# Optimization experiments

Hardware: AMD Instinct MI355X
Metric: run time of the kernel (lower is better)

## Reference

```python
import jax, jax.numpy as jnp
import numpy as np

VOCAB_LIST = np.array([16384, 2048, 256], dtype=np.int64)
SIZES = VOCAB_LIST + 1                       # +1 level-mask token per level
LEVEL_ENDS = jnp.asarray(np.cumsum(SIZES))   # [3] cumulative vocab ends
MASK_TOKENS = LEVEL_ENDS - 1                 # level mask token ids
TOTAL_V = int(SIZES.sum())                   # 18691
N_LAYER, N_EMBD, N_HEAD = 4, 1024, 16
HEAD_DIM = N_EMBD // N_HEAD
FF = 4 * N_EMBD
MEMORY_SPAN = 256
SOFTCAP = 30.0


def rms_norm(x):
    return x * jax.lax.rsqrt(jnp.mean(x * x, axis=-1, keepdims=True) + 1e-6)


def rotary(x):
    # x: [B, S, H, D]; half-split rotation as in modded-nanogpt
    S, D = x.shape[1], x.shape[-1]
    half = D // 2
    inv_freq = 1.0 / (10000.0 ** (jnp.arange(half, dtype=jnp.float32) / half))
    freqs = jnp.outer(jnp.arange(S, dtype=jnp.float32), inv_freq)  # [S, half]
    cos = jnp.cos(freqs)[None, :, None, :]
    sin = jnp.sin(freqs)[None, :, None, :]
    x1, x2 = x[..., :half], x[..., half:]
    return jnp.concatenate([x1 * cos + x2 * sin, -x1 * sin + x2 * cos], axis=-1)


def build_mask(levels):
    # keep kv if causal AND (kv is a higher-level 'global' token OR within recent window)
    S = levels.shape[1]
    q = jnp.arange(S)[:, None]
    k = jnp.arange(S)[None, :]
    causal = q >= k
    recent = (q - k) <= MEMORY_SPAN
    higher = (levels > 0)[:, None, :]                 # [B,1,S]
    return causal[None] & (higher | recent[None])     # [B,S,S]


def forward(idx, target, wte, lambdas, lamb, wq, wk, wv, wo, w1, w2, lm_head):
    B, S = idx.shape
    levels = jnp.searchsorted(LEVEL_ENDS, idx, side='right')   # infer_level
    mask = build_mask(levels)[:, None]                         # [B,1,S,S]
    x = rms_norm(wte[idx])
    x0 = x
    v1 = None
    for i in range(N_LAYER):
        xr = lambdas[i, 0] * x + lambdas[i, 1] * x0
        h = rms_norm(xr)
        q = (h @ wq[i].T).reshape(B, S, N_HEAD, HEAD_DIM)
        k = (h @ wk[i].T).reshape(B, S, N_HEAD, HEAD_DIM)
        v = (h @ wv[i].T).reshape(B, S, N_HEAD, HEAD_DIM)
        if v1 is None:
            v1 = v                                  # value residual from layer 0
        v = (1.0 - lamb[i]) * v + lamb[i] * v1
        q = rotary(rms_norm(q))                     # QK-norm then rotary
        k = rotary(rms_norm(k))
        scores = jnp.einsum('bqhd,bkhd->bhqk', q, k) / jnp.sqrt(jnp.float32(HEAD_DIM))
        scores = jnp.where(mask, scores, -jnp.inf)
        attn = jax.nn.softmax(scores, axis=-1)
        y = jnp.einsum('bhqk,bkhd->bqhd', attn, v).reshape(B, S, N_EMBD)
        x = xr + y @ wo[i].T
        m = rms_norm(x)
        x = x + (jax.nn.relu(m @ w1[i].T) ** 2) @ w2[i].T   # ReLU^2 MLP
    x = rms_norm(x)
    logits = x @ lm_head.T
    logits = SOFTCAP * jnp.tanh(logits / SOFTCAP)
    logp = jax.nn.log_softmax(logits.astype(jnp.float32), axis=-1)
    loss = -jnp.take_along_axis(logp, target[..., None].astype(jnp.int32), axis=-1)[..., 0]
    loss = jnp.where(jnp.isin(target, MASK_TOKENS), 0.0, loss)
    return loss


def setup_inputs() -> dict:
    key = jax.random.key(0)
    ks = jax.random.split(key, 12)
    B, S, D, V, F, L = 2, 2048, N_EMBD, TOTAL_V, FF, N_LAYER
    s = 0.02
    return {
        'idx': jax.random.randint(ks[0], (B, S), 0, V, dtype=jnp.int32),
        'target': jax.random.randint(ks[1], (B, S), 0, V, dtype=jnp.int32),
        'wte': jax.random.normal(ks[2], (V, D), dtype=jnp.float32),
        'lambdas': jnp.tile(jnp.array([1.0, 0.0], dtype=jnp.float32), (L, 1)),
        'lamb': jnp.full((L,), 0.5, dtype=jnp.float32),
        'wq': jax.random.normal(ks[3], (L, D, D), dtype=jnp.float32) * s,
        'wk': jax.random.normal(ks[4], (L, D, D), dtype=jnp.float32) * s,
        'wv': jax.random.normal(ks[5], (L, D, D), dtype=jnp.float32) * s,
        'wo': jax.random.normal(ks[6], (L, D, D), dtype=jnp.float32) * s,
        'w1': jax.random.normal(ks[7], (L, F, D), dtype=jnp.float32) * s,
        'w2': jax.random.normal(ks[8], (L, D, F), dtype=jnp.float32) * s,
        'lm_head': jax.random.normal(ks[9], (V, D), dtype=jnp.float32) * 0.01,
    }


def reference(idx, target, wte, lambdas, lamb, wq, wk, wv, wo, w1, w2, lm_head):
    return forward(idx, target, wte, lambdas, lamb, wq, wk, wv, wo, w1, w2, lm_head)
```

## Files before the change

### kernel.cpp

```cpp
#include <hip/hip_runtime.h>
#include <hip/hip_bf16.h>

#define TT 4096
#define SS 2048
#define BBATCH 2
#define DM 1024
#define NH 16
#define HD 64
#define FFD 4096
#define NL 4
#define VV 18691
#define VP 18816
#define APITCH 72
#define NXLM 147
#define SENT 0x3FFFFFFF

typedef __bf16 bf16x8 __attribute__((ext_vector_type(8)));
typedef float f32x4 __attribute__((ext_vector_type(4)));
typedef const __attribute__((address_space(1))) void* gas_t;
typedef __attribute__((address_space(3))) void* las_t;

__device__ __forceinline__ float bfb2f(unsigned short u) {
    union { unsigned int i; float f; } x;
    x.i = ((unsigned int)u) << 16;
    return x.f;
}
__device__ __forceinline__ unsigned short f2bfb(float f) {
    union { float f; unsigned int i; } x;
    x.f = f;
    unsigned int r = 0x7fffu + ((x.i >> 16) & 1u);
    x.i += r;
    return (unsigned short)(x.i >> 16);
}

__device__ __forceinline__ float wave_sum(float v) {
#pragma unroll
    for (int o = 32; o; o >>= 1) v += __shfl_xor(v, o, 64);
    return v;
}

__device__ __forceinline__ float block_sum256(float v) {
    __shared__ float sb[4];
    v = wave_sum(v);
    int wid = threadIdx.x >> 6;
    if ((threadIdx.x & 63) == 0) sb[wid] = v;
    __syncthreads();
    float t = sb[0] + sb[1] + sb[2] + sb[3];
    __syncthreads();
    return t;
}

__global__ __launch_bounds__(256) void cvtw_kernel(const float* __restrict__ src,
                                                   unsigned short* __restrict__ dst, int n)
{
    int i = (blockIdx.x * 256 + threadIdx.x) * 4;
    if (i >= n) return;
    float4 f = *reinterpret_cast<const float4*>(src + i);
    ushort4 u;
    u.x = f2bfb(f.x); u.y = f2bfb(f.y); u.z = f2bfb(f.z); u.w = f2bfb(f.w);
    *reinterpret_cast<ushort4*>(dst + i) = u;
}

__global__ __launch_bounds__(256) void cvtpad_kernel(const float* __restrict__ src,
                                                     unsigned short* __restrict__ dst,
                                                     int nreal, int ntot)
{
    int i = (blockIdx.x * 256 + threadIdx.x) * 4;
    if (i >= ntot) return;
    ushort4 u = {0, 0, 0, 0};
    if (i < nreal) {
        float4 f = *reinterpret_cast<const float4*>(src + i);
        u.x = f2bfb(f.x); u.y = f2bfb(f.y); u.z = f2bfb(f.z); u.w = f2bfb(f.w);
    }
    *reinterpret_cast<ushort4*>(dst + i) = u;
}

__global__ __launch_bounds__(256) void ropetab_kernel(float2* __restrict__ tab)
{
    int s = blockIdx.x * 8 + (threadIdx.x >> 5);
    int j = threadIdx.x & 31;
    float invf = exp2f(-(float)j * 0.41524101186092025f);
    float ang = (float)s * invf;
    float sn, cs;
    sincosf(ang, &sn, &cs);
    tab[s * 32 + j] = make_float2(cs, sn);
}

__global__ __launch_bounds__(256) void embed_kernel(
    const int* __restrict__ idx, const float* __restrict__ wte,
    float* __restrict__ x, unsigned short* __restrict__ x0, int* __restrict__ levels)
{
    int t = blockIdx.x;
    int id = idx[t];
    const float* row = wte + (size_t)id * DM;
    float4 v = *reinterpret_cast<const float4*>(row + threadIdx.x * 4);
    float ss = v.x * v.x + v.y * v.y + v.z * v.z + v.w * v.w;
    float tot = block_sum256(ss);
    float rs = rsqrtf(tot / (float)DM + 1e-6f);
    float4 o;
    o.x = v.x * rs; o.y = v.y * rs; o.z = v.z * rs; o.w = v.w * rs;
    size_t off = (size_t)t * DM + threadIdx.x * 4;
    *reinterpret_cast<float4*>(x + off) = o;
    ushort4 ub;
    ub.x = f2bfb(o.x); ub.y = f2bfb(o.y); ub.z = f2bfb(o.z); ub.w = f2bfb(o.w);
    *reinterpret_cast<ushort4*>(x0 + off) = ub;
    if (threadIdx.x == 0) levels[t] = (id >= 16385) + (id >= 18434);
}

__global__ __launch_bounds__(256) void pack_kernel(
    const int* __restrict__ levels, int* __restrict__ gpos, int* __restrict__ nbuf)
{
    int b = blockIdx.x;
    const int* lv = levels + b * SS;
    int* gp = gpos + b * SS;
    __shared__ int wsum[4];
    __shared__ int base;
    if (threadIdx.x == 0) base = 0;
    __syncthreads();
    int lane = threadIdx.x & 63, w = threadIdx.x >> 6;
    for (int c = 0; c < SS; c += 256) {
        int s = c + threadIdx.x;
        int flag = (lv[s] > 0) ? 1 : 0;
        unsigned long long mask = __ballot(flag);
        int pre = __popcll(mask & ((1ull << lane) - 1ull));
        int wtot = __popcll(mask);
        if (lane == 0) wsum[w] = wtot;
        __syncthreads();
        int woff = 0;
#pragma unroll
        for (int i = 0; i < 4; ++i) if (i < w) woff += wsum[i];
        int tot = wsum[0] + wsum[1] + wsum[2] + wsum[3];
        int mybase = base;
        if (flag) gp[mybase + woff + pre] = s;
        __syncthreads();
        if (threadIdx.x == 0) base += tot;
        __syncthreads();
    }
    int nb = base;
    int nbp = (nb + 63) & ~63;
    for (int i = nb + threadIdx.x; i < SS; i += 256) gp[i] = SENT;
    if (threadIdx.x == 0) { nbuf[b] = nb; nbuf[BBATCH + b] = nbp; }
}

__global__ __launch_bounds__(64) void gather_kernel(
    const unsigned short* __restrict__ kb, const unsigned short* __restrict__ vb,
    const int* __restrict__ gpos, const int* __restrict__ nbuf,
    unsigned short* __restrict__ kp, unsigned short* __restrict__ vp)
{
    int b = blockIdx.x >> 11;
    int j = blockIdx.x & (SS - 1);
    if (j >= nbuf[BBATCH + b]) return;
    int pos = gpos[b * SS + j];
    int lane = threadIdx.x;
    size_t dst = ((size_t)b * SS + j) * DM + lane * 16;
    if (pos < SS) {
        size_t src = ((size_t)b * SS + pos) * DM + lane * 16;
        *reinterpret_cast<uint4*>(kp + dst) = *reinterpret_cast<const uint4*>(kb + src);
        *reinterpret_cast<uint4*>(kp + dst + 8) = *reinterpret_cast<const uint4*>(kb + src + 8);
        *reinterpret_cast<uint4*>(vp + dst) = *reinterpret_cast<const uint4*>(vb + src);
        *reinterpret_cast<uint4*>(vp + dst + 8) = *reinterpret_cast<const uint4*>(vb + src + 8);
    } else {
        uint4 z = {0, 0, 0, 0};
        *reinterpret_cast<uint4*>(kp + dst) = z;
        *reinterpret_cast<uint4*>(kp + dst + 8) = z;
        *reinterpret_cast<uint4*>(vp + dst) = z;
        *reinterpret_cast<uint4*>(vp + dst + 8) = z;
    }
}

__global__ __launch_bounds__(256) void mixnorm_kernel(
    float* __restrict__ x, const unsigned short* __restrict__ x0,
    const float* __restrict__ lam2, unsigned short* __restrict__ out)
{
    int t = blockIdx.x;
    size_t off = (size_t)t * DM + threadIdx.x * 4;
    float4 xv = *reinterpret_cast<const float4*>(x + off);
    float l0 = lam2[0], l1 = lam2[1];
    ushort4 u = *reinterpret_cast<const ushort4*>(x0 + off);
    float4 r;
    r.x = l0 * xv.x + l1 * bfb2f(u.x);
    r.y = l0 * xv.y + l1 * bfb2f(u.y);
    r.z = l0 * xv.z + l1 * bfb2f(u.z);
    r.w = l0 * xv.w + l1 * bfb2f(u.w);
    float ss = r.x * r.x + r.y * r.y + r.z * r.z + r.w * r.w;
    float tot = block_sum256(ss);
    float rs = rsqrtf(tot / (float)DM + 1e-6f);
    *reinterpret_cast<float4*>(x + off) = r;
    ushort4 ob;
    ob.x = f2bfb(r.x * rs); ob.y = f2bfb(r.y * rs);
    ob.z = f2bfb(r.z * rs); ob.w = f2bfb(r.w * rs);
    *reinterpret_cast<ushort4*>(out + off) = ob;
}

__global__ __launch_bounds__(256) void norm_kernel(
    const float* __restrict__ x, unsigned short* __restrict__ out)
{
    int t = blockIdx.x;
    size_t off = (size_t)t * DM + threadIdx.x * 4;
    float4 r = *reinterpret_cast<const float4*>(x + off);
    float ss = r.x * r.x + r.y * r.y + r.z * r.z + r.w * r.w;
    float tot = block_sum256(ss);
    float rs = rsqrtf(tot / (float)DM + 1e-6f);
    ushort4 ob;
    ob.x = f2bfb(r.x * rs); ob.y = f2bfb(r.y * rs);
    ob.z = f2bfb(r.z * rs); ob.w = f2bfb(r.w * rs);
    *reinterpret_cast<ushort4*>(out + off) = ob;
}

template <int EPI>
__global__ __launch_bounds__(256) void gemm_bb(
    const unsigned short* __restrict__ A, const unsigned short* __restrict__ Bw,
    unsigned short* __restrict__ Cb, float* __restrict__ Cf,
    unsigned short* __restrict__ Kb, unsigned short* __restrict__ Vb,
    const unsigned short* __restrict__ V1in, unsigned short* __restrict__ V1out,
    const float* __restrict__ lambp, const float2* __restrict__ tab,
    int NX, int K, int ldC)
{
    __shared__ unsigned short As[128 * 64];
    __shared__ unsigned short Bs[128 * 64];

    int nwg = gridDim.x;
    int orig = blockIdx.x;
    int qq = nwg >> 3, rr = nwg & 7;
    int xcd = orig & 7, rem = orig >> 3;
    int wg = (xcd < rr ? xcd * (qq + 1) : rr * (qq + 1) + (xcd - rr) * qq) + rem;
    int bx = wg % NX, by = wg / NX;
    int m0 = by * 128, n0 = bx * 128;

    int tid = threadIdx.x, lane = tid & 63, w = tid >> 6;
    int wr = w >> 1, wc = w & 1;
    int rsub = lane >> 3, sl = lane & 7;
    int ssrc = sl ^ rsub;
    int fr = lane & 15, fh = lane >> 4;

    size_t arow[4], brow[4];
#pragma unroll
    for (int i = 0; i < 4; ++i) {
        int c = 4 * w + i;
        arow[i] = (size_t)(m0 + 8 * c + rsub) * K + ssrc * 8;
        brow[i] = (size_t)(n0 + 8 * c + rsub) * K + ssrc * 8;
    }

    f32x4 acc[4][4];
#pragma unroll
    for (int m = 0; m < 4; ++m)
#pragma unroll
        for (int n = 0; n < 4; ++n) acc[m][n] = 0.0f;

    int NT = K >> 6;
    for (int kt = 0; kt < NT; ++kt) {
        int kb = kt * 64;
#pragma unroll
        for (int i = 0; i < 4; ++i) {
            __builtin_amdgcn_global_load_lds((gas_t)(const void*)(A + arow[i] + kb),
                                             (las_t)(void*)(&As[(4 * w + i) * 512]), 16, 0, 0);
            __builtin_amdgcn_global_load_lds((gas_t)(const void*)(Bw + brow[i] + kb),
                                             (las_t)(void*)(&Bs[(4 * w + i) * 512]), 16, 0, 0);
        }
        __syncthreads();
#pragma unroll
        for (int kk = 0; kk < 2; ++kk) {
            int slot = kk * 4 + fh;
            bf16x8 af[4], bfv[4];
#pragma unroll
            for (int m = 0; m < 4; ++m) {
                int row = wr * 64 + m * 16 + fr;
                af[m] = *reinterpret_cast<const bf16x8*>(&As[row * 64 + ((slot ^ (row & 7)) << 3)]);
            }
#pragma unroll
            for (int n = 0; n < 4; ++n) {
                int row = wc * 64 + n * 16 + fr;
                bfv[n] = *reinterpret_cast<const bf16x8*>(&Bs[row * 64 + ((slot ^ (row & 7)) << 3)]);
            }
#pragma unroll
            for (int m = 0; m < 4; ++m)
#pragma unroll
                for (int n = 0; n < 4; ++n)
                    acc[m][n] = __builtin_amdgcn_mfma_f32_16x16x32_bf16(af[m], bfv[n], acc[m][n], 0, 0, 0);
        }
        __syncthreads();
    }

    int rb = m0 + wr * 64 + fh * 4;
    int cb = n0 + wc * 64 + fr;

    if constexpr (EPI == 3) {
        int mat = n0 >> 10;
        if (mat < 2) {
            unsigned short* outp = (mat == 0) ? Cb : Kb;
#pragma unroll
            for (int m = 0; m < 4; ++m) {
#pragma unroll
                for (int j = 0; j < 4; ++j) {
                    int gr = rb + m * 16 + j;
                    int s = gr & (SS - 1);
                    float ss = 0.0f;
#pragma unroll
                    for (int n = 0; n < 4; ++n) ss += acc[m][n][j] * acc[m][n][j];
                    ss += __shfl_xor(ss, 1, 64);
                    ss += __shfl_xor(ss, 2, 64);
                    ss += __shfl_xor(ss, 4, 64);
                    ss += __shfl_xor(ss, 8, 64);
                    float rsn = rsqrtf(ss * (1.0f / (float)HD) + 1e-6f);
                    float nv0 = acc[m][0][j] * rsn;
                    float nv1 = acc[m][1][j] * rsn;
                    float nv2 = acc[m][2][j] * rsn;
                    float nv3 = acc[m][3][j] * rsn;
                    float2 t0 = tab[s * 32 + fr];
                    float2 t1 = tab[s * 32 + fr + 16];
                    float o0 = nv0 * t0.x + nv2 * t0.y;
                    float o1 = nv1 * t1.x + nv3 * t1.y;
                    float o2 = nv2 * t0.x - nv0 * t0.y;
                    float o3 = nv3 * t1.x - nv1 * t1.y;
                    size_t rowo = (size_t)gr * DM + ((cb)&1023);
                    outp[rowo] = f2bfb(o0);
                    outp[rowo + 16] = f2bfb(o1);
                    outp[rowo + 32] = f2bfb(o2);
                    outp[rowo + 48] = f2bfb(o3);
                }
            }
        } else {
            float la = V1out ? 0.0f : *lambp;
#pragma unroll
            for (int n = 0; n < 4; ++n) {
                int gc = cb + n * 16;
#pragma unroll
                for (int m = 0; m < 4; ++m) {
#pragma unroll
                    for (int j = 0; j < 4; ++j) {
                        int gr = rb + m * 16 + j;
                        size_t o = (size_t)gr * DM + (gc & 1023);
                        unsigned short bv = f2bfb(acc[m][n][j]);
                        if (V1out) {
                            Vb[o] = bv;
                            V1out[o] = bv;
                        } else {
                            float mixed = (1.0f - la) * bfb2f(bv) + la * bfb2f(V1in[o]);
                            Vb[o] = f2bfb(mixed);
                        }
                    }
                }
            }
        }
        return;
    }

#pragma unroll
    for (int n = 0; n < 4; ++n) {
        int gc = cb + n * 16;
#pragma unroll
        for (int m = 0; m < 4; ++m) {
#pragma unroll
            for (int j = 0; j < 4; ++j) {
                int gr = rb + m * 16 + j;
                float val = acc[m][n][j];
                if constexpr (EPI == 0) {
                    Cb[(size_t)gr * ldC + gc] = f2bfb(val);
                } else if constexpr (EPI == 1) {
                    float rl = fmaxf(val, 0.0f);
                    Cb[(size_t)gr * ldC + gc] = f2bfb(rl * rl);
                } else if constexpr (EPI == 2) {
                    size_t o = (size_t)gr * ldC + gc;
                    Cf[o] = Cf[o] + val;
                }
            }
        }
    }
}

__global__ __launch_bounds__(256) void gemm_lm(
    const unsigned short* __restrict__ A, const unsigned short* __restrict__ Bw,
    const int* __restrict__ target, float* __restrict__ part, float* __restrict__ zbf,
    int K)
{
    __shared__ unsigned short As[128 * 64];
    __shared__ unsigned short Bs[128 * 64];
    __shared__ float reds[2][2][64];

    int orig = blockIdx.x;
    int xcd = orig & 7, rank = orig >> 3;
    int e = xcd * 588 + rank;
    int g = 0;
#pragma unroll
    for (int it = 0; it < 7; ++it) {
        int sz = (g & 1) ? 584 : 592;
        if (e >= sz) { e -= sz; ++g; }
    }
    int nj = g & 1, mi = g >> 1;
    int bxl = e >> 3, byl = e & 7;
    int bx = nj * 74 + bxl;
    int by = mi * 8 + byl;
    int m0 = by * 128, n0 = bx * 128;

    int tid = threadIdx.x, lane = tid & 63, w = tid >> 6;
    int wr = w >> 1, wc = w & 1;
    int rsub = lane >> 3, sl = lane & 7;
    int ssrc = sl ^ rsub;
    int fr = lane & 15, fh = lane >> 4;

    size_t arow[4], brow[4];
#pragma unroll
    for (int i = 0; i < 4; ++i) {
        int c = 4 * w + i;
        arow[i] = (size_t)(m0 + 8 * c + rsub) * K + ssrc * 8;
        brow[i] = (size_t)(n0 + 8 * c + rsub) * K + ssrc * 8;
    }

    f32x4 acc[4][4];
#pragma unroll
    for (int m = 0; m < 4; ++m)
#pragma unroll
        for (int n = 0; n < 4; ++n) acc[m][n] = 0.0f;

    int NT = K >> 6;
    for (int kt = 0; kt < NT; ++kt) {
        int kb = kt * 64;
#pragma unroll
        for (int i = 0; i < 4; ++i) {
            __builtin_amdgcn_global_load_lds((gas_t)(const void*)(A + arow[i] + kb),
                                             (las_t)(void*)(&As[(4 * w + i) * 512]), 16, 0, 0);
            __builtin_amdgcn_global_load_lds((gas_t)(const void*)(Bw + brow[i] + kb),
                                             (las_t)(void*)(&Bs[(4 * w + i) * 512]), 16, 0, 0);
        }
        __syncthreads();
#pragma unroll
        for (int kk = 0; kk < 2; ++kk) {
            int slot = kk * 4 + fh;
            bf16x8 af[4], bfv[4];
#pragma unroll
            for (int m = 0; m < 4; ++m) {
                int row = wr * 64 + m * 16 + fr;
                af[m] = *reinterpret_cast<const bf16x8*>(&As[row * 64 + ((slot ^ (row & 7)) << 3)]);
            }
#pragma unroll
            for (int n = 0; n < 4; ++n) {
                int row = wc * 64 + n * 16 + fr;
                bfv[n] = *reinterpret_cast<const bf16x8*>(&Bs[row * 64 + ((slot ^ (row & 7)) << 3)]);
            }
#pragma unroll
            for (int m = 0; m < 4; ++m)
#pragma unroll
                for (int n = 0; n < 4; ++n)
                    acc[m][n] = __builtin_amdgcn_mfma_f32_16x16x32_bf16(af[m], bfv[n], acc[m][n], 0, 0, 0);
        }
        __syncthreads();
    }

    int rb = m0 + wr * 64 + fh * 4;
    int cb = n0 + wc * 64 + fr;
#pragma unroll
    for (int m = 0; m < 4; ++m) {
#pragma unroll
        for (int j = 0; j < 4; ++j) {
            int gr = rb + m * 16 + j;
            int tg = target[gr];
            float rs = 0.0f;
#pragma unroll
            for (int n = 0; n < 4; ++n) {
                int gc = cb + n * 16;
                if (gc < VV) {
                    float zv = acc[m][n][j];
                    float tt = __expf(zv * 0.066666667f);
                    rs += __expf(__fdividef(-60.0f, tt + 1.0f));
                    if (gc == tg) zbf[gr] = 30.0f - 60.0f / (tt + 1.0f);
                }
            }
            rs += __shfl_xor(rs, 1, 64);
            rs += __shfl_xor(rs, 2, 64);
            rs += __shfl_xor(rs, 4, 64);
            rs += __shfl_xor(rs, 8, 64);
            if (fr == 0) reds[wr][wc][m * 16 + fh * 4 + j] = rs;
        }
    }
    __syncthreads();
    if (tid < 128) {
        int wrx = tid >> 6, r64 = tid & 63;
        part[(size_t)(m0 + tid) * NXLM + bx] = reds[wrx][0][r64] + reds[wrx][1][r64];
    }
}

__global__ __launch_bounds__(256) void loss_merge_kernel(
    const float* __restrict__ part, const float* __restrict__ zbf,
    const int* __restrict__ target, float* __restrict__ out)
{
    int t = blockIdx.x;
    float l = 0.0f;
    for (int i = threadIdx.x; i < NXLM; i += 256) l += part[(size_t)t * NXLM + i];
    l = block_sum256(l);
    if (threadIdx.x == 0) {
        int tg = target[t];
        float lse = 30.0f + logf(l);
        bool masked = (tg == 16384) || (tg == 18433) || (tg == 18690);
        out[t] = masked ? 0.0f : (lse - zbf[t]);
    }
}

template <int EPI>
__global__ __launch_bounds__(256) void gemm_bb64(
    const unsigned short* __restrict__ A, const unsigned short* __restrict__ Bw,
    unsigned short* __restrict__ Cb, float* __restrict__ Cf,
    int NX, int K, int ldC)
{
    __shared__ unsigned short As[64 * 64];
    __shared__ unsigned short Bs[128 * 64];

    int nwg = gridDim.x;
    int orig = blockIdx.x;
    int qq = nwg >> 3, rr = nwg & 7;
    int xcd = orig & 7, rem = orig >> 3;
    int wg = (xcd < rr ? xcd * (qq + 1) : rr * (qq + 1) + (xcd - rr) * qq) + rem;
    int bx = wg % NX, by = wg / NX;
    int m0 = by * 64, n0 = bx * 128;

    int tid = threadIdx.x, lane = tid & 63, w = tid >> 6;
    int wr = w >> 1, wc = w & 1;
    int rsub = lane >> 3, sl = lane & 7;
    int ssrc = sl ^ rsub;
    int fr = lane & 15, fh = lane >> 4;

    size_t arow[2], brow[4];
#pragma unroll
    for (int i = 0; i < 2; ++i) {
        int c = 2 * w + i;
        arow[i] = (size_t)(m0 + 8 * c + rsub) * K + ssrc * 8;
    }
#pragma unroll
    for (int i = 0; i < 4; ++i) {
        int c = 4 * w + i;
        brow[i] = (size_t)(n0 + 8 * c + rsub) * K + ssrc * 8;
    }

    f32x4 acc[2][4];
#pragma unroll
    for (int m = 0; m < 2; ++m)
#pragma unroll
        for (int n = 0; n < 4; ++n) acc[m][n] = 0.0f;

    int NT = K >> 6;
    for (int kt = 0; kt < NT; ++kt) {
        int kb = kt * 64;
#pragma unroll
        for (int i = 0; i < 2; ++i)
            __builtin_amdgcn_global_load_lds((gas_t)(const void*)(A + arow[i] + kb),
                                             (las_t)(void*)(&As[(2 * w + i) * 512]), 16, 0, 0);
#pragma unroll
        for (int i = 0; i < 4; ++i)
            __builtin_amdgcn_global_load_lds((gas_t)(const void*)(Bw + brow[i] + kb),
                                             (las_t)(void*)(&Bs[(4 * w + i) * 512]), 16, 0, 0);
        __syncthreads();
#pragma unroll
        for (int kk = 0; kk < 2; ++kk) {
            int slot = kk * 4 + fh;
            bf16x8 af[2], bfv[4];
#pragma unroll
            for (int m = 0; m < 2; ++m) {
                int row = wr * 32 + m * 16 + fr;
                af[m] = *reinterpret_cast<const bf16x8*>(&As[row * 64 + ((slot ^ (row & 7)) << 3)]);
            }
#pragma unroll
            for (int n = 0; n < 4; ++n) {
                int row = wc * 64 + n * 16 + fr;
                bfv[n] = *reinterpret_cast<const bf16x8*>(&Bs[row * 64 + ((slot ^ (row & 7)) << 3)]);
            }
#pragma unroll
            for (int m = 0; m < 2; ++m)
#pragma unroll
                for (int n = 0; n < 4; ++n)
                    acc[m][n] = __builtin_amdgcn_mfma_f32_16x16x32_bf16(af[m], bfv[n], acc[m][n], 0, 0, 0);
        }
        __syncthreads();
    }

    int rb = m0 + wr * 32 + fh * 4;
    int cb = n0 + wc * 64 + fr;
#pragma unroll
    for (int n = 0; n < 4; ++n) {
        int gc = cb + n * 16;
#pragma unroll
        for (int m = 0; m < 2; ++m) {
#pragma unroll
            for (int j = 0; j < 4; ++j) {
                int gr = rb + m * 16 + j;
                float val = acc[m][n][j];
                if constexpr (EPI == 0) {
                    Cb[(size_t)gr * ldC + gc] = f2bfb(val);
                } else if constexpr (EPI == 1) {
                    float rl = fmaxf(val, 0.0f);
                    Cb[(size_t)gr * ldC + gc] = f2bfb(rl * rl);
                } else {
                    size_t o = (size_t)gr * ldC + gc;
                    Cf[o] = Cf[o] + val;
                }
            }
        }
    }
}

__global__ __launch_bounds__(256) void attn_mfma_kernel(
    const unsigned short* __restrict__ q, const unsigned short* __restrict__ k,
    const unsigned short* __restrict__ v,
    const unsigned short* __restrict__ kp, const unsigned short* __restrict__ vp,
    const int* __restrict__ gpos, const int* __restrict__ nbuf,
    unsigned short* __restrict__ y)
{
    __shared__ unsigned short Qs[64][APITCH];
    __shared__ unsigned short Ks[64][APITCH];
    __shared__ unsigned short Vt[64][APITCH];
    __shared__ unsigned short Ps[64][APITCH];
    __shared__ int posS[64];

    int bh = blockIdx.x;
    int b = bh >> 4, h = bh & 15;
    int q0 = blockIdx.y * 64;
    size_t base = (size_t)b * SS * DM + h * HD;
    int tid = threadIdx.x;
    int lane = tid & 63, w = tid >> 6;
    int srow = tid >> 2, sc = tid & 3;

    {
        const unsigned short* src = q + base + (size_t)(q0 + srow) * DM;
        *reinterpret_cast<uint4*>(&Qs[srow][sc * 8]) = *reinterpret_cast<const uint4*>(src + sc * 8);
        *reinterpret_cast<uint4*>(&Qs[srow][(sc + 4) * 8]) = *reinterpret_cast<const uint4*>(src + (sc + 4) * 8);
    }
    __syncthreads();

    int fr = lane & 15, fc = (lane >> 4) * 8;
    int rj = (lane >> 4) * 4;

    bf16x8 qa[2];
    qa[0] = *reinterpret_cast<const bf16x8*>(&Qs[w * 16 + fr][fc]);
    qa[1] = *reinterpret_cast<const bf16x8*>(&Qs[w * 16 + fr][32 + fc]);

    float mreg[4], lreg[4];
    f32x4 yacc[4];
#pragma unroll
    for (int j = 0; j < 4; ++j) { mreg[j] = -1e30f; lreg[j] = 0.0f; yacc[j] = 0.0f; }

    int nbp = nbuf[BBATCH + b];

    int t0 = (q0 >= 256) ? ((q0 - 256) >> 6) : 0;
    int t1 = q0 >> 6;
    for (int pass = 0; pass < 2; ++pass) {
        int kt_begin = (pass == 0) ? t0 : 0;
        int kt_end = (pass == 0) ? (t1 + 1) : (nbp >> 6);
        for (int kt = kt_begin; kt < kt_end; ++kt) {
            int k0 = kt * 64;
            if (pass == 1) {
                if (gpos[b * SS + k0] > q0 - 194) break;
            }
            __syncthreads();
            {
                const unsigned short* ksrc = (pass == 0) ? (k + base) : (kp + base);
                const unsigned short* vsrc = (pass == 0) ? (v + base) : (vp + base);
                size_t goff = (size_t)(k0 + srow) * DM;
                uint4 kv0 = *reinterpret_cast<const uint4*>(ksrc + goff + sc * 8);
                uint4 kv1 = *reinterpret_cast<const uint4*>(ksrc + goff + (sc + 4) * 8);
                *reinterpret_cast<uint4*>(&Ks[srow][sc * 8]) = kv0;
                *reinterpret_cast<uint4*>(&Ks[srow][(sc + 4) * 8]) = kv1;
                uint4 vv0 = *reinterpret_cast<const uint4*>(vsrc + goff + sc * 8);
                uint4 vv1 = *reinterpret_cast<const uint4*>(vsrc + goff + (sc + 4) * 8);
                const unsigned short* e0 = reinterpret_cast<const unsigned short*>(&vv0);
                const unsigned short* e1 = reinterpret_cast<const unsigned short*>(&vv1);
#pragma unroll
                for (int i = 0; i < 8; ++i) Vt[sc * 8 + i][srow] = e0[i];
#pragma unroll
                for (int i = 0; i < 8; ++i) Vt[(sc + 4) * 8 + i][srow] = e1[i];
                if (pass == 1 && tid < 64) posS[tid] = gpos[b * SS + k0 + tid];
            }
            __syncthreads();

            f32x4 sacc[4];
#pragma unroll
            for (int n = 0; n < 4; ++n) {
                bf16x8 kb0 = *reinterpret_cast<const bf16x8*>(&Ks[n * 16 + fr][fc]);
                bf16x8 kb1 = *reinterpret_cast<const bf16x8*>(&Ks[n * 16 + fr][32 + fc]);
                f32x4 a = {0.0f, 0.0f, 0.0f, 0.0f};
                a = __builtin_amdgcn_mfma_f32_16x16x32_bf16(qa[0], kb0, a, 0, 0, 0);
                a = __builtin_amdgcn_mfma_f32_16x16x32_bf16(qa[1], kb1, a, 0, 0, 0);
                sacc[n] = a;
            }

            float sm[4][4];
            float cm[4] = {-1e30f, -1e30f, -1e30f, -1e30f};
#pragma unroll
            for (int n = 0; n < 4; ++n) {
                int kg = (pass == 0) ? (k0 + n * 16 + fr) : posS[n * 16 + fr];
#pragma unroll
                for (int j = 0; j < 4; ++j) {
                    int qg = q0 + w * 16 + rj + j;
                    bool valid = (pass == 0) ? ((kg <= qg) && (qg - kg <= 256))
                                             : (kg < qg - 256);
                    float s = valid ? sacc[n][j] * 0.125f : -1e30f;
                    sm[n][j] = s;
                    cm[j] = fmaxf(cm[j], s);
                }
            }
#pragma unroll
            for (int j = 0; j < 4; ++j) {
                cm[j] = fmaxf(cm[j], __shfl_xor(cm[j], 1, 64));
                cm[j] = fmaxf(cm[j], __shfl_xor(cm[j], 2, 64));
                cm[j] = fmaxf(cm[j], __shfl_xor(cm[j], 4, 64));
                cm[j] = fmaxf(cm[j], __shfl_xor(cm[j], 8, 64));
            }
            float sj[4], ps[4];
#pragma unroll
            for (int j = 0; j < 4; ++j) {
                float nm = fmaxf(mreg[j], cm[j]);
                sj[j] = __expf(mreg[j] - nm);
                mreg[j] = nm;
                ps[j] = 0.0f;
            }
#pragma unroll
            for (int n = 0; n < 4; ++n) {
#pragma unroll
                for (int j = 0; j < 4; ++j) {
                    float p = (sm[n][j] > -1e29f) ? __expf(sm[n][j] - mreg[j]) : 0.0f;
                    Ps[w * 16 + rj + j][n * 16 + fr] = f2bfb(p);
                    ps[j] += p;
                }
            }
#pragma unroll
            for (int j = 0; j < 4; ++j) {
                float t = ps[j];
                t += __shfl_xor(t, 1, 64); t += __shfl_xor(t, 2, 64);
                t += __shfl_xor(t, 4, 64); t += __shfl_xor(t, 8, 64);
                lreg[j] = lreg[j] * sj[j] + t;
            }
#pragma unroll
            for (int n = 0; n < 4; ++n)
#pragma unroll
                for (int j = 0; j < 4; ++j) yacc[n][j] *= sj[j];

            bf16x8 pa0 = *reinterpret_cast<const bf16x8*>(&Ps[w * 16 + fr][fc]);
            bf16x8 pa1 = *reinterpret_cast<const bf16x8*>(&Ps[w * 16 + fr][32 + fc]);
#pragma unroll
            for (int n = 0; n < 4; ++n) {
                bf16x8 vb0 = *reinterpret_cast<const bf16x8*>(&Vt[n * 16 + fr][fc]);
                bf16x8 vb1 = *reinterpret_cast<const bf16x8*>(&Vt[n * 16 + fr][32 + fc]);
                yacc[n] = __builtin_amdgcn_mfma_f32_16x16x32_bf16(pa0, vb0, yacc[n], 0, 0, 0);
                yacc[n] = __builtin_amdgcn_mfma_f32_16x16x32_bf16(pa1, vb1, yacc[n], 0, 0, 0);
            }
        }
    }

    float inv[4];
#pragma unroll
    for (int j = 0; j < 4; ++j) inv[j] = 1.0f / lreg[j];
#pragma unroll
    for (int n = 0; n < 4; ++n) {
#pragma unroll
        for (int j = 0; j < 4; ++j) {
            int qg = q0 + w * 16 + rj + j;
            y[base + (size_t)qg * DM + n * 16 + fr] = f2bfb(yacc[n][j] * inv[j]);
        }
    }
}

extern "C" void kernel_launch(void* const* d_in, const int* in_sizes, int n_in,
                              void* d_out, int out_size, void* d_ws, size_t ws_size,
                              hipStream_t stream)
{
    const int* idx = (const int*)d_in[0];
    const int* target = (const int*)d_in[1];
    const float* wte = (const float*)d_in[2];
    const float* lambdas = (const float*)d_in[3];
    const float* lamb = (const float*)d_in[4];
    const float* wq = (const float*)d_in[5];
    const float* wk = (const float*)d_in[6];
    const float* wv = (const float*)d_in[7];
    const float* wo = (const float*)d_in[8];
    const float* w1 = (const float*)d_in[9];
    const float* w2 = (const float*)d_in[10];
    const float* lm_head = (const float*)d_in[11];
    float* out = (float*)d_out;

    char* ws = (char*)d_ws;
    const size_t MB = (size_t)1 << 20;
    float* x            = (float*)(ws);
    unsigned short* x0  = (unsigned short*)(ws + 16 * MB);
    unsigned short* nrm = (unsigned short*)(ws + 24 * MB);
    unsigned short* qb  = (unsigned short*)(ws + 32 * MB);
    unsigned short* kb  = (unsigned short*)(ws + 40 * MB);
    unsigned short* vb  = (unsigned short*)(ws + 48 * MB);
    unsigned short* v1b = (unsigned short*)(ws + 56 * MB);
    unsigned short* yb  = (unsigned short*)(ws + 64 * MB);
    unsigned short* hid = (unsigned short*)(ws + 72 * MB);
    unsigned short* kp  = (unsigned short*)(ws + 72 * MB);
    unsigned short* vp  = (unsigned short*)(ws + 80 * MB);
    float* part         = (float*)(ws + 72 * MB);
    float* zbf          = (float*)(ws + 78 * MB);
    int* levels         = (int*)(ws + 104 * MB);
    int* gpos           = (int*)(ws + 104 * MB + 64 * 1024);
    int* nbuf           = (int*)(ws + 104 * MB + 128 * 1024);
    float2* ropetab     = (float2*)(ws + 104 * MB + 256 * 1024);
    unsigned short* wqkvb = (unsigned short*)(ws + 105 * MB);
    unsigned short* wob = (unsigned short*)(ws + 129 * MB);
    unsigned short* w1b = (unsigned short*)(ws + 137 * MB);
    unsigned short* w2b = (unsigned short*)(ws + 169 * MB);
    unsigned short* lmb = (unsigned short*)(ws + 201 * MB);
    bool cvt = ws_size >= 238 * MB;

    if (cvt) {
        int n1 = DM * DM;
        int nff = NL * FFD * DM;
        for (int i = 0; i < NL; ++i) {
            cvtw_kernel<<<n1 / 1024, 256, 0, stream>>>(wq + (size_t)i * n1, wqkvb + ((size_t)i * 3 + 0) * n1, n1);
            cvtw_kernel<<<n1 / 1024, 256, 0, stream>>>(wk + (size_t)i * n1, wqkvb + ((size_t)i * 3 + 1) * n1, n1);
            cvtw_kernel<<<n1 / 1024, 256, 0, stream>>>(wv + (size_t)i * n1, wqkvb + ((size_t)i * 3 + 2) * n1, n1);
        }
        cvtw_kernel<<<NL * n1 / 1024, 256, 0, stream>>>(wo, wob, NL * n1);
        cvtw_kernel<<<nff / 1024, 256, 0, stream>>>(w1, w1b, nff);
        cvtw_kernel<<<nff / 1024, 256, 0, stream>>>(w2, w2b, nff);
        cvtpad_kernel<<<(VP * DM) / 1024, 256, 0, stream>>>(lm_head, lmb, VV * DM, VP * DM);
    }
    ropetab_kernel<<<SS / 8, 256, 0, stream>>>(ropetab);

    embed_kernel<<<TT, 256, 0, stream>>>(idx, wte, x, x0, levels);
    pack_kernel<<<BBATCH, 256, 0, stream>>>(levels, gpos, nbuf);

    for (int i = 0; i < NL; ++i) {
        mixnorm_kernel<<<TT, 256, 0, stream>>>(x, x0, lambdas + 2 * i, nrm);
        if (cvt) {
            if (i == 0)
                gemm_bb<3><<<768, 256, 0, stream>>>(nrm, wqkvb + (size_t)i * 3 * DM * DM,
                                                    qb, nullptr, kb, vb, nullptr, v1b, nullptr, ropetab, 24, DM, DM);
            else
                gemm_bb<3><<<768, 256, 0, stream>>>(nrm, wqkvb + (size_t)i * 3 * DM * DM,
                                                    qb, nullptr, kb, vb, v1b, nullptr, lamb + i, ropetab, 24, DM, DM);
        }
        gather_kernel<<<BBATCH * SS, 64, 0, stream>>>(kb, vb, gpos, nbuf, kp, vp);
        attn_mfma_kernel<<<dim3(BBATCH * NH, SS / 64), 256, 0, stream>>>(qb, kb, vb, kp, vp, gpos, nbuf, yb);
        if (cvt) {
            gemm_bb64<2><<<512, 256, 0, stream>>>(yb, wob + (size_t)i * DM * DM, nullptr, x, 8, DM, DM);
            norm_kernel<<<TT, 256, 0, stream>>>(x, nrm);
            gemm_bb64<1><<<2048, 256, 0, stream>>>(nrm, w1b + (size_t)i * FFD * DM, hid, nullptr, 32, DM, FFD);
            gemm_bb64<2><<<512, 256, 0, stream>>>(hid, w2b + (size_t)i * DM * FFD, nullptr, x, 8, FFD, DM);
        }
    }

    norm_kernel<<<TT, 256, 0, stream>>>(x, nrm);
    gemm_lm<<<NXLM * 32, 256, 0, stream>>>(nrm, lmb, target, part, zbf, DM);
    loss_merge_kernel<<<TT, 256, 0, stream>>>(part, zbf, target, out);
}
```

Measured before the change: 1.431 ms.

## Split-K the FFN down-projection and fuse its reduction with the next layer's mixnorm

The w2 GEMM (K=4096) is split across two K halves, with 1024 workgroups instead of 512. Each half writes bf16 partials into the q buffer. A new w2mix kernel adds both partials to the residual, applies the next layer's lambda mix and produces the RMS-normed input, which replaces the separate per-layer mixnorm and the final norm. The gather kernel also packs four rows per 256-thread block. In exchange, the partials are rounded to bf16 before accumulation, which adds error, and the pass writes and reads extra partial-sum traffic.

```diff
diff --git a/kernel.cpp b/kernel.cpp
--- a/kernel.cpp
+++ b/kernel.cpp
@@ -142,16 +142,17 @@
     if (threadIdx.x == 0) { nbuf[b] = nb; nbuf[BBATCH + b] = nbp; }
 }
 
-__global__ __launch_bounds__(64) void gather_kernel(
+__global__ __launch_bounds__(256) void gather_kernel(
     const unsigned short* __restrict__ kb, const unsigned short* __restrict__ vb,
     const int* __restrict__ gpos, const int* __restrict__ nbuf,
     unsigned short* __restrict__ kp, unsigned short* __restrict__ vp)
 {
-    int b = blockIdx.x >> 11;
-    int j = blockIdx.x & (SS - 1);
+    int gid = blockIdx.x * 4 + (threadIdx.x >> 6);
+    int b = gid >> 11;
+    int j = gid & (SS - 1);
     if (j >= nbuf[BBATCH + b]) return;
     int pos = gpos[b * SS + j];
-    int lane = threadIdx.x;
+    int lane = threadIdx.x & 63;
     size_t dst = ((size_t)b * SS + j) * DM + lane * 16;
     if (pos < SS) {
         size_t src = ((size_t)b * SS + pos) * DM + lane * 16;
@@ -198,6 +199,39 @@
     int t = blockIdx.x;
     size_t off = (size_t)t * DM + threadIdx.x * 4;
     float4 r = *reinterpret_cast<const float4*>(x + off);
+    float ss = r.x * r.x + r.y * r.y + r.z * r.z + r.w * r.w;
+    float tot = block_sum256(ss);
+    float rs = rsqrtf(tot / (float)DM + 1e-6f);
+    ushort4 ob;
+    ob.x = f2bfb(r.x * rs); ob.y = f2bfb(r.y * rs);
+    ob.z = f2bfb(r.z * rs); ob.w = f2bfb(r.w * rs);
+    *reinterpret_cast<ushort4*>(out + off) = ob;
+}
+
+__global__ __launch_bounds__(256) void w2mix_kernel(
+    float* __restrict__ x, const unsigned short* __restrict__ p0,
+    const unsigned short* __restrict__ p1, const unsigned short* __restrict__ x0,
+    const float* __restrict__ lam2, unsigned short* __restrict__ out, int domix)
+{
+    int t = blockIdx.x;
+    size_t off = (size_t)t * DM + threadIdx.x * 4;
+    float4 xv = *reinterpret_cast<const float4*>(x + off);
+    ushort4 a = *reinterpret_cast<const ushort4*>(p0 + off);
+    ushort4 b = *reinterpret_cast<const ushort4*>(p1 + off);
+    float4 r;
+    r.x = xv.x + bfb2f(a.x) + bfb2f(b.x);
+    r.y = xv.y + bfb2f(a.y) + bfb2f(b.y);
+    r.z = xv.z + bfb2f(a.z) + bfb2f(b.z);
+    r.w = xv.w + bfb2f(a.w) + bfb2f(b.w);
+    if (domix) {
+        float l0 = lam2[0], l1 = lam2[1];
+        ushort4 u = *reinterpret_cast<const ushort4*>(x0 + off);
+        r.x = l0 * r.x + l1 * bfb2f(u.x);
+        r.y = l0 * r.y + l1 * bfb2f(u.y);
+        r.z = l0 * r.z + l1 * bfb2f(u.z);
+        r.w = l0 * r.w + l1 * bfb2f(u.w);
+        *reinterpret_cast<float4*>(x + off) = r;
+    }
     float ss = r.x * r.x + r.y * r.y + r.z * r.z + r.w * r.w;
     float tot = block_sum256(ss);
     float rs = rsqrtf(tot / (float)DM + 1e-6f);
@@ -495,7 +529,7 @@
     }
 }
 
-template <int EPI>
+template <int EPI, int KS = 1>
 __global__ __launch_bounds__(256) void gemm_bb64(
     const unsigned short* __restrict__ A, const unsigned short* __restrict__ Bw,
     unsigned short* __restrict__ Cb, float* __restrict__ Cf,
@@ -509,8 +543,13 @@
     int qq = nwg >> 3, rr = nwg & 7;
     int xcd = orig & 7, rem = orig >> 3;
     int wg = (xcd < rr ? xcd * (qq + 1) : rr * (qq + 1) + (xcd - rr) * qq) + rem;
-    int bx = wg % NX, by = wg / NX;
+    int per = nwg / KS;
+    int ks = (KS == 1) ? 0 : (wg / per);
+    int rem2 = (KS == 1) ? wg : (wg % per);
+    int bx = rem2 % NX, by = rem2 / NX;
     int m0 = by * 64, n0 = bx * 128;
+    int KSUB = K / KS;
+    int kbase = ks * KSUB;
 
     int tid = threadIdx.x, lane = tid & 63, w = tid >> 6;
     int wr = w >> 1, wc = w & 1;
@@ -536,9 +575,9 @@
 #pragma unroll
         for (int n = 0; n < 4; ++n) acc[m][n] = 0.0f;
 
-    int NT = K >> 6;
+    int NT = KSUB >> 6;
     for (int kt = 0; kt < NT; ++kt) {
-        int kb = kt * 64;
+        int kb = kbase + kt * 64;
 #pragma unroll
         for (int i = 0; i < 2; ++i)
             __builtin_amdgcn_global_load_lds((gas_t)(const void*)(A + arow[i] + kb),
@@ -587,9 +626,11 @@
                 } else if constexpr (EPI == 1) {
                     float rl = fmaxf(val, 0.0f);
                     Cb[(size_t)gr * ldC + gc] = f2bfb(rl * rl);
-                } else {
+                } else if constexpr (EPI == 2) {
                     size_t o = (size_t)gr * ldC + gc;
                     Cf[o] = Cf[o] + val;
+                } else {
+                    Cb[(size_t)ks * ((size_t)TT * DM) + (size_t)gr * ldC + gc] = f2bfb(val);
                 }
             }
         }
@@ -789,6 +830,7 @@
     unsigned short* vp  = (unsigned short*)(ws + 80 * MB);
     float* part         = (float*)(ws + 72 * MB);
     float* zbf          = (float*)(ws + 78 * MB);
+    unsigned short* w2p = qb;
     int* levels         = (int*)(ws + 104 * MB);
     int* gpos           = (int*)(ws + 104 * MB + 64 * 1024);
     int* nbuf           = (int*)(ws + 104 * MB + 128 * 1024);
@@ -817,9 +859,9 @@
 
     embed_kernel<<<TT, 256, 0, stream>>>(idx, wte, x, x0, levels);
     pack_kernel<<<BBATCH, 256, 0, stream>>>(levels, gpos, nbuf);
+    mixnorm_kernel<<<TT, 256, 0, stream>>>(x, x0, lambdas, nrm);
 
     for (int i = 0; i < NL; ++i) {
-        mixnorm_kernel<<<TT, 256, 0, stream>>>(x, x0, lambdas + 2 * i, nrm);
         if (cvt) {
             if (i == 0)
                 gemm_bb<3><<<768, 256, 0, stream>>>(nrm, wqkvb + (size_t)i * 3 * DM * DM,
@@ -828,17 +870,22 @@
                 gemm_bb<3><<<768, 256, 0, stream>>>(nrm, wqkvb + (size_t)i * 3 * DM * DM,
                                                     qb, nullptr, kb, vb, v1b, nullptr, lamb + i, ropetab, 24, DM, DM);
         }
-        gather_kernel<<<BBATCH * SS, 64, 0, stream>>>(kb, vb, gpos, nbuf, kp, vp);
+        gather_kernel<<<BBATCH * SS / 4, 256, 0, stream>>>(kb, vb, gpos, nbuf, kp, vp);
         attn_mfma_kernel<<<dim3(BBATCH * NH, SS / 64), 256, 0, stream>>>(qb, kb, vb, kp, vp, gpos, nbuf, yb);
         if (cvt) {
             gemm_bb64<2><<<512, 256, 0, stream>>>(yb, wob + (size_t)i * DM * DM, nullptr, x, 8, DM, DM);
             norm_kernel<<<TT, 256, 0, stream>>>(x, nrm);
             gemm_bb64<1><<<2048, 256, 0, stream>>>(nrm, w1b + (size_t)i * FFD * DM, hid, nullptr, 32, DM, FFD);
-            gemm_bb64<2><<<512, 256, 0, stream>>>(hid, w2b + (size_t)i * DM * FFD, nullptr, x, 8, FFD, DM);
-        }
-    }
-
-    norm_kernel<<<TT, 256, 0, stream>>>(x, nrm);
+            gemm_bb64<4, 2><<<1024, 256, 0, stream>>>(hid, w2b + (size_t)i * DM * FFD, w2p, nullptr, 8, FFD, DM);
+            if (i < NL - 1)
+                w2mix_kernel<<<TT, 256, 0, stream>>>(x, w2p, w2p + (size_t)TT * DM, x0,
+                                                     lambdas + 2 * (i + 1), nrm, 1);
+            else
+                w2mix_kernel<<<TT, 256, 0, stream>>>(x, w2p, w2p + (size_t)TT * DM, x0,
+                                                     nullptr, nrm, 0);
+        }
+    }
+
     gemm_lm<<<NXLM * 32, 256, 0, stream>>>(nrm, lmb, target, part, zbf, DM);
     loss_merge_kernel<<<TT, 256, 0, stream>>>(part, zbf, target, out);
 }
```

Measured after the change: 1.306 ms. 8.7% less time.
